# Optimization experiments

Hardware: AMD Instinct MI355X
Metric: run time of the kernel (lower is better)

Reference implementation:

```python
import jax, jax.numpy as jnp
import numpy as np

EPS = 1e-5

def channel_norm(x):
    # per-(batch,channel) norm over spatial dims; torch.var default is unbiased (ddof=1)
    mn = x.mean(axis=(-1, -2), keepdims=True)
    std = jnp.sqrt(x.var(axis=(-1, -2), keepdims=True, ddof=1) + EPS)
    return (x - mn) / std

def conv1x1(x, W, b):
    # x: [B,C,H,W], W: [O,C], b: [O]
    return jnp.einsum('oc,bchw->bohw', W, x) + b[None, :, None, None]

def setup_inputs() -> dict:
    key = jax.random.key(0)
    ks = jax.random.split(key, 10)
    B, C, H, W = 4, 512, 64, 64
    s = 1.0 / np.sqrt(C)  # kaiming-uniform-ish scale for 1x1 conv
    inp = {
        'f_c': jax.random.normal(ks[0], (B, C, H, W), jnp.float32),
        'f_s': jax.random.normal(ks[1], (B, C, H, W), jnp.float32),
        'W_c1': jax.random.uniform(ks[2], (C, C), jnp.float32, -s, s),
        'b_c1': jax.random.uniform(ks[3], (C,), jnp.float32, -s, s),
        'W_s1': jax.random.uniform(ks[4], (C, C), jnp.float32, -s, s),
        'b_s1': jax.random.uniform(ks[5], (C,), jnp.float32, -s, s),
        'W_s2': jax.random.uniform(ks[6], (C, C), jnp.float32, -s, s),
        'b_s2': jax.random.uniform(ks[7], (C,), jnp.float32, -s, s),
        'W_csc': jax.random.uniform(ks[8], (C, C), jnp.float32, -s, s),
        'b_csc': jax.random.uniform(ks[9], (C,), jnp.float32, -s, s),
    }
    return inp

def reference(f_c, f_s, W_c1, b_c1, W_s1, b_s1, W_s2, b_s2, W_csc, b_csc):
    B, C, H, W = f_c.shape
    f_c_hat = channel_norm(f_c)
    f_s_hat = channel_norm(f_s)
    f = conv1x1(f_c_hat, W_c1, b_c1).reshape(B, C, H * W)  # queries [B,C,N]
    g = conv1x1(f_s_hat, W_s1, b_s1).reshape(B, C, H * W)  # keys    [B,C,N]
    scores = jnp.einsum('bci,bcj->bij', f, g)              # [B,N,N]
    attention = jax.nn.softmax(scores, axis=-1)
    h = conv1x1(f_s_hat, W_s2, b_s2).reshape(B, C, H * W)  # values  [B,C,N]
    out = jnp.einsum('bcj,bij->bci', h, attention).reshape(B, C, H, W)
    return conv1x1(out, W_csc, b_csc) + f_c
```

## Files before the change

kernel.cpp:

```cpp
#include <hip/hip_runtime.h>

typedef unsigned short u16;
typedef __attribute__((ext_vector_type(8))) _Float16 f16x8;
typedef __attribute__((ext_vector_type(16))) float f32x16;

#define N_SP 4096
#define C_CH 512
#define B_SZ 4

struct PtrTab { u16* p[4]; };

__device__ __forceinline__ u16 f2h(float f) {
    union { _Float16 h; u16 u; } x; x.h = (_Float16)f; return x.u;
}
__device__ __forceinline__ float h2f(u16 u) {
    union { u16 u; _Float16 h; } x; x.u = u; return (float)x.h;
}
__device__ __forceinline__ void async_cp16(const void* g, void* l) {
    __builtin_amdgcn_global_load_lds((const __attribute__((address_space(1))) unsigned*)g,
                                     (__attribute__((address_space(3))) unsigned*)l, 16, 0, 0);
}
__device__ __forceinline__ float wave_reduce_sum(float v) {
    #pragma unroll
    for (int off = 32; off; off >>= 1) v += __shfl_xor(v, off, 64);
    return v;
}
__device__ __forceinline__ float wave_reduce_max(float v) {
    #pragma unroll
    for (int off = 32; off; off >>= 1) v = fmaxf(v, __shfl_xor(v, off, 64));
    return v;
}
__device__ __forceinline__ void bar() { asm volatile("s_barrier" ::: "memory"); }
template<int N> __device__ __forceinline__ void vmwait() {
    if constexpr (N == 0)  asm volatile("s_waitcnt vmcnt(0)" ::: "memory");
    else if constexpr (N == 4)  asm volatile("s_waitcnt vmcnt(4)" ::: "memory");
    else if constexpr (N == 6)  asm volatile("s_waitcnt vmcnt(6)" ::: "memory");
    else if constexpr (N == 8)  asm volatile("s_waitcnt vmcnt(8)" ::: "memory");
    else if constexpr (N == 12) asm volatile("s_waitcnt vmcnt(12)" ::: "memory");
}

__global__ __launch_bounds__(256) void transpose_cast_stats(
        const float* __restrict__ fc, const float* __restrict__ fs,
        u16* __restrict__ xc, u16* __restrict__ xs,
        float* __restrict__ part_s, float* __restrict__ part_ss) {
    __shared__ float tile[64][65];
    const int t = threadIdx.x;
    const int n0 = blockIdx.x * 64, c0 = blockIdx.y * 64;
    const int z = blockIdx.z;
    const int b = z & 3, which = z >> 2;
    const float* src = which ? fs : fc;
    u16* dst = which ? xs : xc;
    const int r = t >> 4, q4 = (t & 15) * 4;
    #pragma unroll
    for (int it = 0; it < 4; ++it) {
        const int row = it * 16 + r;
        float4 v = *(const float4*)(src + ((size_t)b * C_CH + c0 + row) * N_SP + n0 + q4);
        tile[row][q4 + 0] = v.x; tile[row][q4 + 1] = v.y;
        tile[row][q4 + 2] = v.z; tile[row][q4 + 3] = v.w;
    }
    __syncthreads();
    {
        const int cr = t >> 2, q = t & 3;
        float s = 0.f, ss = 0.f;
        #pragma unroll
        for (int i = 0; i < 16; ++i) {
            float a = tile[cr][q * 16 + i];
            s += a; ss += a * a;
        }
        s += __shfl_xor(s, 1, 64);  s += __shfl_xor(s, 2, 64);
        ss += __shfl_xor(ss, 1, 64); ss += __shfl_xor(ss, 2, 64);
        if (q == 0) {
            atomicAdd(&part_s[z * 512 + c0 + cr], s);
            atomicAdd(&part_ss[z * 512 + c0 + cr], ss);
        }
    }
    #pragma unroll
    for (int it = 0; it < 4; ++it) {
        const int nrow = it * 16 + r;
        ushort4 h4;
        h4.x = f2h(tile[q4 + 0][nrow]);
        h4.y = f2h(tile[q4 + 1][nrow]);
        h4.z = f2h(tile[q4 + 2][nrow]);
        h4.w = f2h(tile[q4 + 3][nrow]);
        *(ushort4*)(dst + ((size_t)b * N_SP + n0 + nrow) * C_CH + c0 + q4) = h4;
    }
}

__global__ __launch_bounds__(256) void prep1(
        const float* __restrict__ W_c1, const float* __restrict__ W_s1,
        const float* __restrict__ W_s2, const float* __restrict__ W_csc,
        const float* __restrict__ b_c1, const float* __restrict__ b_s2,
        const float* __restrict__ b_csc,
        u16* __restrict__ Wbase,
        const float* __restrict__ part_s, const float* __restrict__ part_ss,
        float* __restrict__ mu_a, float* __restrict__ rs_a,
        float* __restrict__ w_u, float* __restrict__ bfold0) {
    __shared__ float tile[64][65];
    const int t = threadIdx.x, z = blockIdx.z;
    if (z < 4) {
        const int n0 = blockIdx.x * 64, c0 = blockIdx.y * 64;
        const float* W = (z == 0) ? W_c1 : (z == 1) ? W_s1 : (z == 2) ? W_s2 : W_csc;
        u16* D = Wbase + ((z == 0) ? 2 : (z == 1) ? 0 : (z == 2) ? 3 : 1) * 262144;
        const int r = t >> 4, q4 = (t & 15) * 4;
        #pragma unroll
        for (int it = 0; it < 4; ++it) {
            const int row = it * 16 + r;
            float4 v = *(const float4*)(W + (size_t)(c0 + row) * 512 + n0 + q4);
            if (z == 3) {
                ushort4 h4 = { f2h(v.x), f2h(v.y), f2h(v.z), f2h(v.w) };
                *(ushort4*)(D + (size_t)(c0 + row) * 512 + n0 + q4) = h4;
            } else {
                tile[row][q4 + 0] = v.x; tile[row][q4 + 1] = v.y;
                tile[row][q4 + 2] = v.z; tile[row][q4 + 3] = v.w;
            }
        }
        __syncthreads();
        if (z == 3) return;
        #pragma unroll
        for (int it = 0; it < 4; ++it) {
            const int nrow = it * 16 + r;
            ushort4 h4;
            h4.x = f2h(tile[q4 + 0][nrow]);
            h4.y = f2h(tile[q4 + 1][nrow]);
            h4.z = f2h(tile[q4 + 2][nrow]);
            h4.w = f2h(tile[q4 + 3][nrow]);
            *(ushort4*)(D + (size_t)(n0 + nrow) * 512 + c0 + q4) = h4;
        }
        return;
    }
    const int flat = blockIdx.y * 8 + blockIdx.x;
    if (flat < 8) {
        #pragma unroll
        for (int h = 0; h < 2; ++h) {
            const int c = flat * 512 + h * 256 + t;
            const float S = part_s[c], SS = part_ss[c];
            const float mean = S * (1.f / N_SP);
            const float var = (SS - S * mean) * (1.f / (N_SP - 1));
            mu_a[c] = mean;
            rs_a[c] = rsqrtf(var + 1e-5f);
        }
    } else if (flat < 10) {
        const int d = (flat - 8) * 256 + t;
        float acc = 0.f;
        for (int o = 0; o < 512; ++o) acc += b_c1[o] * W_s1[(size_t)o * 512 + d];
        w_u[d] = acc;
    } else if (flat < 42) {
        const int w4 = t >> 6, l = t & 63;
        #pragma unroll
        for (int q = 0; q < 4; ++q) {
            const int o = (flat - 10) * 16 + w4 * 4 + q;
            const float4 w0 = *(const float4*)(W_csc + (size_t)o * 512 + l * 8);
            const float4 w1 = *(const float4*)(W_csc + (size_t)o * 512 + l * 8 + 4);
            const float4 b0 = *(const float4*)(b_s2 + l * 8);
            const float4 b1 = *(const float4*)(b_s2 + l * 8 + 4);
            float acc = w0.x * b0.x + w0.y * b0.y + w0.z * b0.z + w0.w * b0.w
                      + w1.x * b1.x + w1.y * b1.y + w1.z * b1.z + w1.w * b1.w;
            acc = wave_reduce_sum(acc);
            if (l == 0) bfold0[o] = acc + b_csc[o];
        }
    }
}

__global__ __launch_bounds__(256) void prep2(
        const u16* __restrict__ WqT16, const u16* __restrict__ Wf16,
        const u16* __restrict__ xs,
        const float* __restrict__ mu_a, const float* __restrict__ rs_a,
        const float* __restrict__ bfold0, const float* __restrict__ w_u,
        u16* __restrict__ Wq_z, u16* __restrict__ Wf_z,
        float* __restrict__ bq, float* __restrict__ bh, float* __restrict__ u_) {
    const int id = blockIdx.x, t = threadIdx.x;
    if (id < 1024) {
        const int y = id >> 9;
        const size_t e = ((size_t)(id & 511) * 256 + t) * 8;
        const int z = (int)(e >> 18), rem = (int)(e & 262143);
        const int d = rem >> 9, a0 = rem & 511;
        u16 v[8];
        if (y == 0) {
            *(uint4*)v = *(const uint4*)(WqT16 + rem);
            const float rd = rs_a[(4 + z) * 512 + d];
            const float* rc = rs_a + z * 512 + a0;
            #pragma unroll
            for (int i = 0; i < 8; ++i) v[i] = f2h(h2f(v[i]) * rc[i] * rd);
            *(uint4*)(Wq_z + e) = *(const uint4*)v;
        } else {
            *(uint4*)v = *(const uint4*)(Wf16 + rem);
            const float* rk = rs_a + (4 + z) * 512 + a0;
            #pragma unroll
            for (int i = 0; i < 8; ++i) v[i] = f2h(h2f(v[i]) * rk[i]);
            *(uint4*)(Wf_z + e) = *(const uint4*)v;
        }
    } else if (id < 2048) {
        const int w = t >> 6, l = t & 63;
        const int oid = (id - 1024) * 4 + w;
        const int kind = oid >> 11;
        const int z = (oid >> 9) & 3, d = oid & 511;
        const u16* row = (kind == 0 ? WqT16 : Wf16) + (size_t)d * 512;
        const int sb = (kind == 0 ? z : 4 + z) * 512;
        float acc = 0.f;
        #pragma unroll
        for (int i = 0; i < 8; ++i) {
            const int a = l * 8 + i;
            acc += h2f(row[a]) * mu_a[sb + a] * rs_a[sb + a];
        }
        acc = wave_reduce_sum(acc);
        if (l == 0) {
            if (kind == 0) bq[z * 512 + d] = -acc * rs_a[(4 + z) * 512 + d];
            else           bh[z * 512 + d] = bfold0[d] - acc;
        }
    } else {
        const int id2 = id - 2048;
        const int b = id2 >> 6, xblk = id2 & 63;
        const int w = t >> 6, l = t & 63;
        float4 u0 = *(const float4*)(w_u + l * 8);
        float4 u1 = *(const float4*)(w_u + l * 8 + 4);
        const float4 r0 = *(const float4*)(rs_a + (4 + b) * 512 + l * 8);
        const float4 r1 = *(const float4*)(rs_a + (4 + b) * 512 + l * 8 + 4);
        u0.x *= r0.x; u0.y *= r0.y; u0.z *= r0.z; u0.w *= r0.w;
        u1.x *= r1.x; u1.y *= r1.y; u1.z *= r1.z; u1.w *= r1.w;
        #pragma unroll
        for (int jj = 0; jj < 16; ++jj) {
            const int j = xblk * 64 + w * 16 + jj;
            const u16* row = xs + ((size_t)b * N_SP + j) * C_CH + l * 8;
            f16x8 x = *(const f16x8*)row;
            float acc = (float)x[0] * u0.x + (float)x[1] * u0.y + (float)x[2] * u0.z + (float)x[3] * u0.w
                      + (float)x[4] * u1.x + (float)x[5] * u1.y + (float)x[6] * u1.z + (float)x[7] * u1.w;
            acc = wave_reduce_sum(acc);
            if (l == 0) u_[(size_t)b * N_SP + j] = acc;
        }
    }
}

enum { OUT_F32 = 0, OUT_F16 = 1 };

template<int OUTMODE, bool TABB, bool TABD, int MI, int MJ>
__global__ __launch_bounds__(256) void gemm_bt(
    const u16* __restrict__ A, const u16* __restrict__ B, PtrTab tab,
    float* __restrict__ Df, u16* __restrict__ Dh,
    const float* __restrict__ bias_m, const float* __restrict__ bias_n,
    const float* __restrict__ res,
    int M, int N, int K, int lda, int ldb, int ldd,
    size_t sA, size_t sB, size_t sD, size_t sR, int sBm, int sBn)
{
    constexpr int TM = MI * 64, TN = MJ * 64, BK = 64;
    constexpr int AITS = (TM * BK) / (256 * 8);
    constexpr int BITS = (TN * BK) / (256 * 8);
    __shared__ u16 smem[(TM + TN) * BK];
    u16* As = smem;
    u16* Bs = smem + TM * BK;

    const int t = threadIdx.x;
    const int l = t & 63, w = t >> 6;
    const int m0 = blockIdx.y * TM, n0 = blockIdx.x * TN;
    const size_t zb = blockIdx.z;
    const u16* pA = A + zb * sA + (size_t)m0 * lda;
    const u16* pB = (TABB ? tab.p[zb] : B + zb * sB) + (size_t)n0 * ldb;

    const int wr = (w & 1) * (MI * 32), wc = (w >> 1) * (MJ * 32);

    f32x16 acc[MI][MJ] = {};

    for (int k0 = 0; k0 < K; k0 += BK) {
        #pragma unroll
        for (int it = 0; it < AITS; ++it) {
            const int L = it * 256 + t;
            const int row = L >> 3, c = L & 7;
            const int sc = (c ^ (row & 7)) * 8;
            async_cp16(pA + (size_t)row * lda + k0 + sc, As + L * 8);
        }
        #pragma unroll
        for (int it = 0; it < BITS; ++it) {
            const int L = it * 256 + t;
            const int row = L >> 3, c = L & 7;
            const int sc = (c ^ (row & 7)) * 8;
            async_cp16(pB + (size_t)row * ldb + k0 + sc, Bs + L * 8);
        }
        __syncthreads();
        #pragma unroll
        for (int kk = 0; kk < 4; ++kk) {
            f16x8 af[MI], bf[MJ];
            #pragma unroll
            for (int i = 0; i < MI; ++i) {
                const int row = wr + i * 32 + (l & 31);
                const int ch = ((kk * 2 + (l >> 5)) ^ (row & 7)) * 8;
                af[i] = *(const f16x8*)(As + row * BK + ch);
            }
            #pragma unroll
            for (int j = 0; j < MJ; ++j) {
                const int row = wc + j * 32 + (l & 31);
                const int ch = ((kk * 2 + (l >> 5)) ^ (row & 7)) * 8;
                bf[j] = *(const f16x8*)(Bs + row * BK + ch);
            }
            #pragma unroll
            for (int i = 0; i < MI; ++i)
                #pragma unroll
                for (int j = 0; j < MJ; ++j)
                    acc[i][j] = __builtin_amdgcn_mfma_f32_32x32x16_f16(af[i], bf[j], acc[i][j], 0, 0, 0);
        }
        __syncthreads();
    }

    const int cl = l & 31, rh = (l >> 5) * 4;
    u16* pDh = (OUTMODE == OUT_F16) ? (TABD ? tab.p[zb] : Dh + zb * sD) : nullptr;
    float* pDf = (OUTMODE == OUT_F32) ? (Df + zb * sD) : nullptr;
    #pragma unroll
    for (int i = 0; i < MI; ++i) {
        #pragma unroll
        for (int j = 0; j < MJ; ++j) {
            const int nn = n0 + wc + j * 32 + cl;
            const float bn = bias_n ? bias_n[(size_t)sBn * zb + nn] : 0.f;
            #pragma unroll
            for (int reg = 0; reg < 16; ++reg) {
                const int ml = (reg & 3) + 8 * (reg >> 2) + rh;
                const int mm = m0 + wr + i * 32 + ml;
                float v = acc[i][j][reg] + bn;
                if (bias_m) v += bias_m[(size_t)sBm * zb + mm];
                const size_t off = (size_t)mm * ldd + nn;
                if (OUTMODE == OUT_F32) {
                    if (res) v += res[zb * sR + off];
                    pDf[off] = v;
                } else {
                    pDh[off] = f2h(v);
                }
            }
        }
    }
}

template<int OUTMODE, bool TABB, bool TABD, int BM, int BN>
__global__ __launch_bounds__(512, 2) void gemm_db(
    const u16* __restrict__ A, const u16* __restrict__ B, PtrTab tab,
    float* __restrict__ Df, u16* __restrict__ Dh,
    const float* __restrict__ bias_n, const float* __restrict__ res,
    int K, int lda, int ldb, int ldd,
    size_t sA, size_t sB, size_t sD, size_t sR, int sBn)
{
    constexpr int BK = 64;
    constexpr int AITS = (BM * BK) / (512 * 8);
    constexpr int BITS = (BN * BK) / (512 * 8);
    constexpr int LTOT = AITS + BITS;
    constexpr int LDSH = (BM + BN) * BK;
    constexpr int MI_W = BM / 64;
    constexpr int NJ_W = BN / 128;
    __shared__ u16 smem[2 * LDSH];

    const int t = threadIdx.x;
    const int l = t & 63, w = t >> 6;
    const int m0 = blockIdx.y * BM, n0 = blockIdx.x * BN;
    const size_t zb = blockIdx.z;
    const u16* pA = A + zb * sA + (size_t)m0 * lda;
    const u16* pB = (TABB ? tab.p[zb] : B + zb * sB) + (size_t)n0 * ldb;

    const int wmo = (w & 1) * (BM / 2);
    const int wno = (w >> 1) * (BN / 4);

    f32x16 acc[MI_W][NJ_W] = {};

    auto stage = [&](int buf, int k0) {
        u16* As_ = smem + buf * LDSH;
        u16* Bs_ = As_ + BM * BK;
        #pragma unroll
        for (int it = 0; it < AITS; ++it) {
            const int L = it * 512 + t;
            const int row = L >> 3, c = L & 7;
            const int sc = (c ^ (row & 7)) * 8;
            async_cp16(pA + (size_t)row * lda + k0 + sc, As_ + L * 8);
        }
        #pragma unroll
        for (int it = 0; it < BITS; ++it) {
            const int L = it * 512 + t;
            const int row = L >> 3, c = L & 7;
            const int sc = (c ^ (row & 7)) * 8;
            async_cp16(pB + (size_t)row * ldb + k0 + sc, Bs_ + L * 8);
        }
    };

    const int NT = K / BK;
    stage(0, 0);
    for (int tl = 0; tl < NT; ++tl) {
        bar();
        if (tl + 1 < NT) {
            stage((tl + 1) & 1, (tl + 1) * BK);
            vmwait<LTOT>();
        } else {
            vmwait<0>();
        }
        bar();
        const u16* As = smem + (tl & 1) * LDSH;
        const u16* Bs = As + BM * BK;
        #pragma unroll
        for (int kk = 0; kk < 4; ++kk) {
            f16x8 af[MI_W], bf[NJ_W];
            #pragma unroll
            for (int i = 0; i < MI_W; ++i) {
                const int row = wmo + i * 32 + (l & 31);
                const int ch = ((kk * 2 + (l >> 5)) ^ (row & 7)) * 8;
                af[i] = *(const f16x8*)(As + row * BK + ch);
            }
            #pragma unroll
            for (int j = 0; j < NJ_W; ++j) {
                const int row = wno + j * 32 + (l & 31);
                const int ch = ((kk * 2 + (l >> 5)) ^ (row & 7)) * 8;
                bf[j] = *(const f16x8*)(Bs + row * BK + ch);
            }
            __builtin_amdgcn_s_setprio(1);
            #pragma unroll
            for (int i = 0; i < MI_W; ++i)
                #pragma unroll
                for (int j = 0; j < NJ_W; ++j)
                    acc[i][j] = __builtin_amdgcn_mfma_f32_32x32x16_f16(af[i], bf[j], acc[i][j], 0, 0, 0);
            __builtin_amdgcn_s_setprio(0);
        }
    }

    const int cl = l & 31, rh = (l >> 5) * 4;
    u16* pDh = (OUTMODE == OUT_F16) ? (TABD ? tab.p[zb] : Dh + zb * sD) : nullptr;
    float* pDf = (OUTMODE == OUT_F32) ? (Df + zb * sD) : nullptr;
    #pragma unroll
    for (int i = 0; i < MI_W; ++i) {
        #pragma unroll
        for (int j = 0; j < NJ_W; ++j) {
            const int nn = n0 + wno + j * 32 + cl;
            const float bn = bias_n ? bias_n[(size_t)sBn * zb + nn] : 0.f;
            #pragma unroll
            for (int reg = 0; reg < 16; ++reg) {
                const int ml = (reg & 3) + 8 * (reg >> 2) + rh;
                const int mm = m0 + wmo + i * 32 + ml;
                float v = acc[i][j][reg] + bn;
                const size_t off = (size_t)mm * ldd + nn;
                if (OUTMODE == OUT_F32) {
                    if (res) v += res[zb * sR + off];
                    pDf[off] = v;
                } else {
                    pDh[off] = f2h(v);
                }
            }
        }
    }
}

__global__ __launch_bounds__(256) void softmax_kernel(PtrTab tab) {
    u16* row = tab.p[blockIdx.y] + (size_t)blockIdx.x * N_SP;
    const int t = threadIdx.x;
    u16 raw[16];
    *(uint4*)(raw + 0) = *(const uint4*)(row + t * 16);
    *(uint4*)(raw + 8) = *(const uint4*)(row + t * 16 + 8);
    float v[16];
    float mx = -1e30f;
    #pragma unroll
    for (int i = 0; i < 16; ++i) { v[i] = h2f(raw[i]); mx = fmaxf(mx, v[i]); }
    mx = wave_reduce_max(mx);
    __shared__ float red[4];
    const int wave = t >> 6;
    if ((t & 63) == 0) red[wave] = mx;
    __syncthreads();
    mx = fmaxf(fmaxf(red[0], red[1]), fmaxf(red[2], red[3]));
    float sum = 0.f;
    #pragma unroll
    for (int i = 0; i < 16; ++i) { v[i] = __expf(v[i] - mx); sum += v[i]; }
    sum = wave_reduce_sum(sum);
    __syncthreads();
    if ((t & 63) == 0) red[wave] = sum;
    __syncthreads();
    const float inv = 1.f / (red[0] + red[1] + red[2] + red[3]);
    #pragma unroll
    for (int i = 0; i < 16; ++i) raw[i] = f2h(v[i] * inv);
    *(uint4*)(row + t * 16)     = *(const uint4*)(raw + 0);
    *(uint4*)(row + t * 16 + 8) = *(const uint4*)(raw + 8);
}

extern "C" void kernel_launch(void* const* d_in, const int* in_sizes, int n_in,
                              void* d_out, int out_size, void* d_ws, size_t ws_size,
                              hipStream_t stream) {
    const float* f_c   = (const float*)d_in[0];
    const float* f_s   = (const float*)d_in[1];
    const float* W_c1  = (const float*)d_in[2];
    const float* b_c1  = (const float*)d_in[3];
    const float* W_s1  = (const float*)d_in[4];
    const float* b_s1  = (const float*)d_in[5]; (void)b_s1;
    const float* W_s2  = (const float*)d_in[6];
    const float* b_s2  = (const float*)d_in[7];
    const float* W_csc = (const float*)d_in[8];
    const float* b_csc = (const float*)d_in[9];

    const size_t PB = (size_t)N_SP * C_CH;
    const size_t M1 = 1024 * 1024;

    u16* ws   = (u16*)d_ws;
    u16* Xs   = ws;
    u16* q_   = ws + 8 * M1;
    u16* hc   = ws + 16 * M1;
    u16* Xc   = ws + 24 * M1;
    u16* S3   = ws + 24 * M1;
    u16* S0   = ws + 40 * M1;
    u16* S1   = ws + 56 * M1;
    u16* S2   = ws + 72 * M1;
    u16* Wbase= ws + 88 * M1;
    u16* WqT16= Wbase + 4 * 262144;
    u16* Wf16 = Wbase + 5 * 262144;
    u16* Wq_z = Wbase + 6 * 262144;
    u16* Wf_z = Wq_z + 1048576;
    float* f32b = (float*)(ws + 92 * M1);
    float* part_s  = f32b;
    float* part_ss = f32b + 4096;
    float* mu_a    = f32b + 8192;
    float* rs_a    = f32b + 12288;
    float* w_u     = f32b + 16384;
    float* bfold0  = f32b + 16896;
    float* bq      = f32b + 17408;
    float* bh      = f32b + 19456;
    float* u_      = f32b + 21504;

    PtrTab Stab; Stab.p[0] = S0; Stab.p[1] = S1; Stab.p[2] = S2; Stab.p[3] = S3;
    PtrTab tab0 = Stab;

    hipMemsetAsync(part_s, 0, 2 * 4096 * sizeof(float), stream);

    transpose_cast_stats<<<dim3(64, 8, 8), 256, 0, stream>>>(f_c, f_s, Xc, Xs, part_s, part_ss);

    prep1<<<dim3(8, 8, 5), 256, 0, stream>>>(W_c1, W_s1, W_s2, W_csc, b_c1, b_s2, b_csc,
                                             Wbase, part_s, part_ss, mu_a, rs_a, w_u, bfold0);

    gemm_bt<OUT_F16, false, false, 2, 2><<<dim3(4, 4, 2), 256, 0, stream>>>(
        Wbase, Wbase + 2 * 262144, tab0, nullptr, WqT16, nullptr, nullptr, nullptr,
        512, 512, 512, 512, 512, 512, 262144, 262144, 262144, 0, 0, 0);

    prep2<<<2304, 256, 0, stream>>>(WqT16, Wf16, Xs, mu_a, rs_a, bfold0, w_u,
                                    Wq_z, Wf_z, bq, bh, u_);

    gemm_bt<OUT_F16, false, false, 1, 2><<<dim3(4, 64, B_SZ), 256, 0, stream>>>(
        Xc, Wq_z, tab0, nullptr, q_, nullptr, bq, nullptr,
        N_SP, C_CH, C_CH, C_CH, C_CH, C_CH, PB, 262144, PB, 0, 0, 512);
    gemm_bt<OUT_F16, false, false, 1, 2><<<dim3(32, 8, B_SZ), 256, 0, stream>>>(
        Wf_z, Xs, tab0, nullptr, hc, bh, nullptr, nullptr,
        C_CH, N_SP, C_CH, C_CH, C_CH, N_SP, 262144, PB, PB, 0, 512, 0);

    gemm_db<OUT_F16, false, true, 256, 256><<<dim3(16, 16, B_SZ), 512, 0, stream>>>(
        q_, Xs, Stab, nullptr, nullptr, u_, nullptr,
        C_CH, C_CH, C_CH, N_SP, PB, PB, 0, 0, N_SP);

    softmax_kernel<<<dim3(N_SP, B_SZ), 256, 0, stream>>>(Stab);

    gemm_db<OUT_F32, true, false, 128, 256><<<dim3(16, 4, B_SZ), 512, 0, stream>>>(
        hc, nullptr, Stab, (float*)d_out, nullptr, nullptr, f_c,
        N_SP, N_SP, N_SP, N_SP, PB, 0, PB, PB, 0);
}
```

Before: 443.3 us.

## Replace double-buffered GEMM with quadrant-phased prefetch pipeline and XCD-aware block remap

The double-buffered GEMM is rewritten as a four-phase loop over output quadrants. Each phase issues one quarter of the next K-tile's async loads (A or B half) while MFMAs run on the current tile, with barriers and waitcnts placed between phases. Block indices are remapped so consecutive blocks land on the same XCD for better L2 reuse. The two projection GEMMs now use this kernel instead of the smaller gemm_bt. The risks are more barriers per K-step and the fact that correctness depends on the fragile vmcnt counts.

```diff
diff --git a/kernel.cpp b/kernel.cpp
--- a/kernel.cpp
+++ b/kernel.cpp
@@ -33,10 +33,11 @@
 __device__ __forceinline__ void bar() { asm volatile("s_barrier" ::: "memory"); }
 template<int N> __device__ __forceinline__ void vmwait() {
     if constexpr (N == 0)  asm volatile("s_waitcnt vmcnt(0)" ::: "memory");
+    else if constexpr (N == 2)  asm volatile("s_waitcnt vmcnt(2)" ::: "memory");
+    else if constexpr (N == 3)  asm volatile("s_waitcnt vmcnt(3)" ::: "memory");
     else if constexpr (N == 4)  asm volatile("s_waitcnt vmcnt(4)" ::: "memory");
     else if constexpr (N == 6)  asm volatile("s_waitcnt vmcnt(6)" ::: "memory");
     else if constexpr (N == 8)  asm volatile("s_waitcnt vmcnt(8)" ::: "memory");
-    else if constexpr (N == 12) asm volatile("s_waitcnt vmcnt(12)" ::: "memory");
 }
 
 __global__ __launch_bounds__(256) void transpose_cast_stats(
@@ -327,111 +328,141 @@
 }
 
 template<int OUTMODE, bool TABB, bool TABD, int BM, int BN>
-__global__ __launch_bounds__(512, 2) void gemm_db(
+__global__ __launch_bounds__(512, 2) void gemm_p8(
     const u16* __restrict__ A, const u16* __restrict__ B, PtrTab tab,
     float* __restrict__ Df, u16* __restrict__ Dh,
-    const float* __restrict__ bias_n, const float* __restrict__ res,
+    const float* __restrict__ bias_m, const float* __restrict__ bias_n,
+    const float* __restrict__ res,
     int K, int lda, int ldb, int ldd,
-    size_t sA, size_t sB, size_t sD, size_t sR, int sBn)
+    size_t sA, size_t sB, size_t sD, size_t sR, int sBm, int sBn)
 {
     constexpr int BK = 64;
-    constexpr int AITS = (BM * BK) / (512 * 8);
-    constexpr int BITS = (BN * BK) / (512 * 8);
-    constexpr int LTOT = AITS + BITS;
     constexpr int LDSH = (BM + BN) * BK;
-    constexpr int MI_W = BM / 64;
-    constexpr int NJ_W = BN / 128;
+    constexpr int MI_Q = BM / 128;
+    constexpr int LA = BM / 128, LB = BN / 128;
+    constexpr int WN = LA + LB;
+    static_assert(BN == 256, "col mapping assumes BN=256");
     __shared__ u16 smem[2 * LDSH];
 
     const int t = threadIdx.x;
     const int l = t & 63, w = t >> 6;
-    const int m0 = blockIdx.y * BM, n0 = blockIdx.x * BN;
+
+    const int gx = gridDim.x, nxy = gx * gridDim.y;
+    const int orig = blockIdx.x + gx * blockIdx.y;
+    const int wg = (orig & 7) * (nxy >> 3) + (orig >> 3);
+    const int m0 = (wg / gx) * BM, n0 = (wg % gx) * BN;
+
     const size_t zb = blockIdx.z;
     const u16* pA = A + zb * sA + (size_t)m0 * lda;
     const u16* pB = (TABB ? tab.p[zb] : B + zb * sB) + (size_t)n0 * ldb;
 
-    const int wmo = (w & 1) * (BM / 2);
-    const int wno = (w >> 1) * (BN / 4);
-
-    f32x16 acc[MI_W][NJ_W] = {};
-
-    auto stage = [&](int buf, int k0) {
-        u16* As_ = smem + buf * LDSH;
-        u16* Bs_ = As_ + BM * BK;
-        #pragma unroll
-        for (int it = 0; it < AITS; ++it) {
+    f32x16 acc[2][2][MI_Q] = {};
+
+    auto stageA = [&](int buf, int k0, int rh) {
+        u16* dst = smem + buf * LDSH;
+        #pragma unroll
+        for (int it = 0; it < LA; ++it) {
             const int L = it * 512 + t;
-            const int row = L >> 3, c = L & 7;
+            const int row = rh * (BM / 2) + (L >> 3), c = L & 7;
             const int sc = (c ^ (row & 7)) * 8;
-            async_cp16(pA + (size_t)row * lda + k0 + sc, As_ + L * 8);
-        }
-        #pragma unroll
-        for (int it = 0; it < BITS; ++it) {
+            async_cp16(pA + (size_t)row * lda + k0 + sc, dst + row * BK + c * 8);
+        }
+    };
+    auto stageB = [&](int buf, int k0, int rh) {
+        u16* dst = smem + buf * LDSH + BM * BK;
+        #pragma unroll
+        for (int it = 0; it < LB; ++it) {
             const int L = it * 512 + t;
-            const int row = L >> 3, c = L & 7;
+            const int row = rh * (BN / 2) + (L >> 3), c = L & 7;
             const int sc = (c ^ (row & 7)) * 8;
-            async_cp16(pB + (size_t)row * ldb + k0 + sc, Bs_ + L * 8);
+            async_cp16(pB + (size_t)row * ldb + k0 + sc, dst + row * BK + c * 8);
         }
     };
 
     const int NT = K / BK;
-    stage(0, 0);
+    stageA(0, 0, 0); stageB(0, 0, 0); stageA(0, 0, 1); stageB(0, 0, 1);
+    vmwait<WN>();
+    bar();
+
     for (int tl = 0; tl < NT; ++tl) {
-        bar();
-        if (tl + 1 < NT) {
-            stage((tl + 1) & 1, (tl + 1) * BK);
-            vmwait<LTOT>();
-        } else {
-            vmwait<0>();
-        }
-        bar();
-        const u16* As = smem + (tl & 1) * LDSH;
+        const int cur = tl & 1, nxt = cur ^ 1;
+        const u16* As = smem + cur * LDSH;
         const u16* Bs = As + BM * BK;
-        #pragma unroll
-        for (int kk = 0; kk < 4; ++kk) {
-            f16x8 af[MI_W], bf[NJ_W];
-            #pragma unroll
-            for (int i = 0; i < MI_W; ++i) {
-                const int row = wmo + i * 32 + (l & 31);
+        const int k1 = (tl + 1) * BK;
+        const bool pf = (tl + 1 < NT);
+
+        #pragma unroll
+        for (int ph = 0; ph < 4; ++ph) {
+            constexpr int QI[4] = {0, 1, 1, 0};
+            constexpr int QJ[4] = {0, 0, 1, 1};
+            const int qi = QI[ph], qj = QJ[ph];
+            const int rbase = qi * (BM / 2) + (w & 1) * (BM / 4);
+            const int cbase = qj * (BN / 2) + (w >> 1) * (BN / 8);
+
+            f16x8 af[MI_Q][4], bf[4];
+            #pragma unroll
+            for (int fi = 0; fi < MI_Q; ++fi)
+                #pragma unroll
+                for (int kk = 0; kk < 4; ++kk) {
+                    const int row = rbase + fi * 32 + (l & 31);
+                    const int ch = ((kk * 2 + (l >> 5)) ^ (row & 7)) * 8;
+                    af[fi][kk] = *(const f16x8*)(As + row * BK + ch);
+                }
+            #pragma unroll
+            for (int kk = 0; kk < 4; ++kk) {
+                const int row = cbase + (l & 31);
                 const int ch = ((kk * 2 + (l >> 5)) ^ (row & 7)) * 8;
-                af[i] = *(const f16x8*)(As + row * BK + ch);
-            }
-            #pragma unroll
-            for (int j = 0; j < NJ_W; ++j) {
-                const int row = wno + j * 32 + (l & 31);
-                const int ch = ((kk * 2 + (l >> 5)) ^ (row & 7)) * 8;
-                bf[j] = *(const f16x8*)(Bs + row * BK + ch);
-            }
+                bf[kk] = *(const f16x8*)(Bs + row * BK + ch);
+            }
+
+            if (pf) {
+                if      (ph == 0) stageA(nxt, k1, 0);
+                else if (ph == 1) stageB(nxt, k1, 0);
+                else if (ph == 2) stageA(nxt, k1, 1);
+                else              stageB(nxt, k1, 1);
+            }
+            if (ph == 0) { if (pf) vmwait<WN>(); else vmwait<0>(); }
+            else if ((ph == 1 || ph == 3) && pf) vmwait<WN>();
+
+            bar();
+            asm volatile("s_waitcnt lgkmcnt(0)" ::: "memory");
+            __builtin_amdgcn_sched_barrier(0);
             __builtin_amdgcn_s_setprio(1);
             #pragma unroll
-            for (int i = 0; i < MI_W; ++i)
+            for (int fi = 0; fi < MI_Q; ++fi)
                 #pragma unroll
-                for (int j = 0; j < NJ_W; ++j)
-                    acc[i][j] = __builtin_amdgcn_mfma_f32_32x32x16_f16(af[i], bf[j], acc[i][j], 0, 0, 0);
+                for (int kk = 0; kk < 4; ++kk)
+                    acc[qi][qj][fi] = __builtin_amdgcn_mfma_f32_32x32x16_f16(
+                        af[fi][kk], bf[kk], acc[qi][qj][fi], 0, 0, 0);
             __builtin_amdgcn_s_setprio(0);
-        }
-    }
-
-    const int cl = l & 31, rh = (l >> 5) * 4;
+            bar();
+        }
+    }
+
+    const int cl = l & 31, rhh = (l >> 5) * 4;
     u16* pDh = (OUTMODE == OUT_F16) ? (TABD ? tab.p[zb] : Dh + zb * sD) : nullptr;
     float* pDf = (OUTMODE == OUT_F32) ? (Df + zb * sD) : nullptr;
     #pragma unroll
-    for (int i = 0; i < MI_W; ++i) {
-        #pragma unroll
-        for (int j = 0; j < NJ_W; ++j) {
-            const int nn = n0 + wno + j * 32 + cl;
-            const float bn = bias_n ? bias_n[(size_t)sBn * zb + nn] : 0.f;
-            #pragma unroll
-            for (int reg = 0; reg < 16; ++reg) {
-                const int ml = (reg & 3) + 8 * (reg >> 2) + rh;
-                const int mm = m0 + wmo + i * 32 + ml;
-                float v = acc[i][j][reg] + bn;
-                const size_t off = (size_t)mm * ldd + nn;
-                if (OUTMODE == OUT_F32) {
-                    if (res) v += res[zb * sR + off];
-                    pDf[off] = v;
-                } else {
-                    pDh[off] = f2h(v);
+    for (int qi = 0; qi < 2; ++qi) {
+        #pragma unroll
+        for (int qj = 0; qj < 2; ++qj) {
+            #pragma unroll
+            for (int fi = 0; fi < MI_Q; ++fi) {
+                const int nn = n0 + qj * (BN / 2) + (w >> 1) * (BN / 8) + cl;
+                const float bn = bias_n ? bias_n[(size_t)sBn * zb + nn] : 0.f;
+                #pragma unroll
+                for (int reg = 0; reg < 16; ++reg) {
+                    const int ml = (reg & 3) + 8 * (reg >> 2) + rhh;
+                    const int mm = m0 + qi * (BM / 2) + (w & 1) * (BM / 4) + fi * 32 + ml;
+                    float v = acc[qi][qj][fi][reg] + bn;
+                    if (bias_m) v += bias_m[(size_t)sBm * zb + mm];
+                    const size_t off = (size_t)mm * ldd + nn;
+                    if (OUTMODE == OUT_F32) {
+                        if (res) v += res[zb * sR + off];
+                        pDf[off] = v;
+                    } else {
+                        pDh[off] = f2h(v);
+                    }
                 }
             }
         }
@@ -527,20 +558,20 @@
     prep2<<<2304, 256, 0, stream>>>(WqT16, Wf16, Xs, mu_a, rs_a, bfold0, w_u,
                                     Wq_z, Wf_z, bq, bh, u_);
 
-    gemm_bt<OUT_F16, false, false, 1, 2><<<dim3(4, 64, B_SZ), 256, 0, stream>>>(
+    gemm_p8<OUT_F16, false, false, 128, 256><<<dim3(2, 32, B_SZ), 512, 0, stream>>>(
         Xc, Wq_z, tab0, nullptr, q_, nullptr, bq, nullptr,
-        N_SP, C_CH, C_CH, C_CH, C_CH, C_CH, PB, 262144, PB, 0, 0, 512);
-    gemm_bt<OUT_F16, false, false, 1, 2><<<dim3(32, 8, B_SZ), 256, 0, stream>>>(
+        C_CH, C_CH, C_CH, C_CH, PB, 262144, PB, 0, 0, 512);
+    gemm_p8<OUT_F16, false, false, 128, 256><<<dim3(16, 4, B_SZ), 512, 0, stream>>>(
         Wf_z, Xs, tab0, nullptr, hc, bh, nullptr, nullptr,
-        C_CH, N_SP, C_CH, C_CH, C_CH, N_SP, 262144, PB, PB, 0, 512, 0);
-
-    gemm_db<OUT_F16, false, true, 256, 256><<<dim3(16, 16, B_SZ), 512, 0, stream>>>(
-        q_, Xs, Stab, nullptr, nullptr, u_, nullptr,
-        C_CH, C_CH, C_CH, N_SP, PB, PB, 0, 0, N_SP);
+        C_CH, C_CH, C_CH, N_SP, 262144, PB, PB, 0, 512, 0);
+
+    gemm_p8<OUT_F16, false, true, 256, 256><<<dim3(16, 16, B_SZ), 512, 0, stream>>>(
+        q_, Xs, Stab, nullptr, nullptr, nullptr, u_, nullptr,
+        C_CH, C_CH, C_CH, N_SP, PB, PB, 0, 0, 0, N_SP);
 
     softmax_kernel<<<dim3(N_SP, B_SZ), 256, 0, stream>>>(Stab);
 
-    gemm_db<OUT_F32, true, false, 128, 256><<<dim3(16, 4, B_SZ), 512, 0, stream>>>(
-        hc, nullptr, Stab, (float*)d_out, nullptr, nullptr, f_c,
-        N_SP, N_SP, N_SP, N_SP, PB, 0, PB, PB, 0);
-}
+    gemm_p8<OUT_F32, true, false, 128, 256><<<dim3(16, 4, B_SZ), 512, 0, stream>>>(
+        hc, nullptr, Stab, (float*)d_out, nullptr, nullptr, nullptr, f_c,
+        N_SP, N_SP, N_SP, N_SP, PB, 0, PB, PB, 0, 0);
+}
```

Result: slower. 475.5 us (+7.3%).
